# Performance work log

Measured on AMD Instinct MI355X. Metric: run time of the kernel, lower is better.

## Reference

```python
import jax, jax.numpy as jnp
import numpy as np

C = 4          # num_components
B = 2          # true batch
HEADS = 24
DIM_HEAD = 64
D = HEADS * DIM_HEAD      # 1536, attn.out_dim == query dim
CROSS = 2048              # encoder hidden dim
S = 2048                  # latent sequence length
E = 77                    # encoder sequence length
PAD = 77                  # pad_length (must equal E for the broadcast in the original code)


def setup_inputs() -> dict:
    key = jax.random.key(0)
    ks = jax.random.split(key, 12)
    w = 0.02
    return {
        "hidden_states": jax.random.normal(ks[0], (B * C, S, D), jnp.float32),
        "encoder_hidden_states": jax.random.normal(ks[1], (B * C, E, CROSS), jnp.float32),
        "Wq": jax.random.normal(ks[2], (D, D), jnp.float32) * w,
        "bq": jax.random.normal(ks[3], (D,), jnp.float32) * w,
        "Wk": jax.random.normal(ks[4], (D, CROSS), jnp.float32) * w,
        "bk": jax.random.normal(ks[5], (D,), jnp.float32) * w,
        "Wv": jax.random.normal(ks[6], (D, CROSS), jnp.float32) * w,
        "bv": jax.random.normal(ks[7], (D,), jnp.float32) * w,
        "Wo": jax.random.normal(ks[8], (D, D), jnp.float32) * w,
        "bo": jax.random.normal(ks[9], (D,), jnp.float32) * w,
        "pad_length": PAD,
    }


def reference(hidden_states, encoder_hidden_states, Wq, bq, Wk, bk, Wv, bv, Wo, bo, pad_length):
    BC, S_, D_ = hidden_states.shape
    E_ = encoder_hidden_states.shape[1]
    Bsz = BC // C
    scale = 1.0 / np.sqrt(DIM_HEAD)

    # projections (torch nn.Linear: x @ W.T + b)
    q = hidden_states @ Wq.T + bq                      # [BC, S, D]
    k = encoder_hidden_states @ Wk.T + bk              # [BC, E, D]
    v = encoder_hidden_states @ Wv.T + bv              # [BC, E, D]
    # pad branch: to_k/to_v applied to zeros -> just the bias, broadcast over pad tokens
    k_pad = jnp.broadcast_to(bk, (BC, pad_length, D_))  # [BC, PAD, D]
    v_pad = jnp.broadcast_to(bv, (BC, pad_length, D_))
    v = jnp.concatenate([v, v_pad], axis=1)            # [BC, E+PAD, D]

    # split heads
    qh = q.reshape(BC, S_, HEADS, DIM_HEAD)
    kh = k.reshape(BC, E_, HEADS, DIM_HEAD)
    kph = k_pad.reshape(BC, pad_length, HEADS, DIM_HEAD)
    vh = v.reshape(BC, E_ + pad_length, HEADS, DIM_HEAD)

    # scores: [BC, H, S, E] and [BC, H, S, PAD]
    scores = jnp.einsum("bihd,bjhd->bhij", qh, kh) * scale
    scores_pad = jnp.einsum("bihd,bjhd->bhij", qh, kph) * scale

    # component-wise softmax: view as [C, B, H, S, *], softmax over component axis 0
    scores = scores.reshape(C, Bsz, HEADS, S_, E_)
    scores_pad = scores_pad.reshape(C, Bsz, HEADS, S_, pad_length)
    w_main = jax.nn.softmax(scores, axis=0)
    w_pad = jax.nn.softmax(scores_pad, axis=0) * (C / pad_length) * (1.0 - w_main)

    w_main = w_main.reshape(BC, HEADS, S_, E_)
    w_pad = w_pad.reshape(BC, HEADS, S_, pad_length)
    weights = jnp.concatenate([w_main, w_pad], axis=-1)  # [BC, H, S, E+PAD]

    # attention @ V -> merge heads
    out = jnp.einsum("bhij,bjhd->bihd", weights, vh).reshape(BC, S_, D_)
    out = out @ Wo.T + bo   # to_out[0]; dropout is identity in eval
    return out
```

## Files before the change

### kernel.cpp

```cpp
#include <hip/hip_runtime.h>
#include <hip/hip_bf16.h>


typedef __attribute__((ext_vector_type(8))) short short8;
typedef __attribute__((ext_vector_type(4))) float f32x4;
typedef __attribute__((ext_vector_type(4))) _Float16 half4;

#define DEV __device__ __forceinline__

DEV ushort f2bf(float x) {
  __hip_bfloat16 h = __float2bfloat16(x);
  return *reinterpret_cast<ushort*>(&h);
}


__global__ __launch_bounds__(256) void cvt_all(const float* __restrict__ hs, ushort* __restrict__ hs_bf,
                                               const float* __restrict__ Wq, ushort* __restrict__ Wq_bf,
                                               const float* __restrict__ Wk, ushort* __restrict__ Wk_bf,
                                               const float* __restrict__ Wv, ushort* __restrict__ Wv_bf,
                                               const float* __restrict__ Wo, ushort* __restrict__ Wo_bf,
                                               const float* __restrict__ ehs, ushort* __restrict__ ehs_bf) {
  const int b0 = 6291456;
  const int b1 = b0 + 589824;
  const int b2 = b1 + 786432;
  const int b3 = b2 + 786432;
  const int b4 = b3 + 589824;
  const int total = b4 + 327680;
  int idx = blockIdx.x * blockDim.x + threadIdx.x;
  int stride = gridDim.x * blockDim.x;
  for (int q = idx; q < total; q += stride) {
    const float* in; ushort* out; int qq;
    bool zero = false;
    if (q < b0)      { in = hs;  out = hs_bf;  qq = q; }
    else if (q < b1) { in = Wq;  out = Wq_bf;  qq = q - b0; }
    else if (q < b2) { in = Wk;  out = Wk_bf;  qq = q - b1; }
    else if (q < b3) { in = Wv;  out = Wv_bf;  qq = q - b2; }
    else if (q < b4) { in = Wo;  out = Wo_bf;  qq = q - b3; }
    else {
      qq = q - b4;
      int r = qq >> 9;
      in = ehs; out = ehs_bf;
      zero = (r >= 616);
    }
    ushort4 o;
    if (!zero) {
      float4 f = reinterpret_cast<const float4*>(in)[qq];
      o.x = f2bf(f.x); o.y = f2bf(f.y); o.z = f2bf(f.z); o.w = f2bf(f.w);
    } else {
      o.x = 0; o.y = 0; o.z = 0; o.w = 0;
    }
    reinterpret_cast<ushort4*>(out)[qq] = o;
  }
}


template <typename OutT>
DEV void gemm_body(const ushort* __restrict__ A, const ushort* __restrict__ B,
                   const float* __restrict__ bias, OutT* __restrict__ C,
                   int M, int N, int K) {
  __shared__ __align__(16) ushort lds[32768];
  const int tid = threadIdx.x;
  const int lane = tid & 63;
  const int wid = tid >> 6;
  const int wr = wid >> 1, wc = wid & 1;

  const int nwg = gridDim.x * gridDim.y;
  const int lin = blockIdx.y * gridDim.x + blockIdx.x;
  const int q8 = nwg >> 3, r8 = nwg & 7;
  const int xcd = lin & 7, i8 = lin >> 3;
  const int swl = (xcd < r8 ? xcd * (q8 + 1) : r8 * (q8 + 1) + (xcd - r8) * q8) + i8;
  const long m0 = (long)(swl / gridDim.y) * 128;
  const long n0 = (long)(swl % gridDim.y) * 128;

  const int ll = lane & 15, g = lane >> 4;
  const int swz = ll & 7;

  const int srow = wid * 8 + (lane >> 3);
  const int scol = ((lane & 7) ^ (lane >> 3)) * 8;
  const ushort* pa = A + (m0 + srow) * (long)K + scol;
  const ushort* pb = B + (n0 + srow) * (long)K + scol;
  const long qstep = 32 * (long)K;

  f32x4 acc[4][4] = {};

#define STAGE(tt, bsel)                                                                    \
  do {                                                                                     \
    const long kt_ = (long)(tt) * 64;                                                      \
    const int ab_ = (bsel) * 32768 + wid * 1024;                                           \
    _Pragma("unroll") for (int q = 0; q < 4; ++q)                                          \
        __builtin_amdgcn_global_load_lds(                                                  \
            (const __attribute__((address_space(1))) void*)(pa + kt_ + q * qstep),         \
            (__attribute__((address_space(3))) void*)((char*)lds + ab_ + q * 4096),        \
            16, 0, 0);                                                                     \
    _Pragma("unroll") for (int q = 0; q < 4; ++q)                                          \
        __builtin_amdgcn_global_load_lds(                                                  \
            (const __attribute__((address_space(1))) void*)(pb + kt_ + q * qstep),         \
            (__attribute__((address_space(3))) void*)((char*)lds + ab_ + 16384 + q * 4096),\
            16, 0, 0);                                                                     \
  } while (0)

  const int nt = K >> 6;
  STAGE(0, 0);
  STAGE(1, 1);
  asm volatile("s_waitcnt vmcnt(8)" ::: "memory");
  __builtin_amdgcn_s_barrier();

  for (int t = 0; t < nt; ++t) {
    const int buf = t & 1;
    const char* abase = (const char*)lds + buf * 32768;
    const char* bbase = abase + 16384;
    short8 af[4][2], bfr[4][2];
#pragma unroll
    for (int m = 0; m < 4; ++m)
#pragma unroll
      for (int ks = 0; ks < 2; ++ks)
        af[m][ks] = *reinterpret_cast<const short8*>(
            abase + (wr * 64 + m * 16 + ll) * 128 + (((ks * 4 + g) ^ swz) * 16));
#pragma unroll
    for (int n = 0; n < 4; ++n)
#pragma unroll
      for (int ks = 0; ks < 2; ++ks)
        bfr[n][ks] = *reinterpret_cast<const short8*>(
            bbase + (wc * 64 + n * 16 + ll) * 128 + (((ks * 4 + g) ^ swz) * 16));
    asm volatile("s_waitcnt lgkmcnt(0)" ::: "memory");
    __builtin_amdgcn_s_barrier();

    if (t < nt - 2) {
      STAGE(t + 2, buf);
      asm volatile("s_waitcnt vmcnt(8)" ::: "memory");
    } else if (t == nt - 2) {
      asm volatile("s_waitcnt vmcnt(0)" ::: "memory");
    }
    __builtin_amdgcn_sched_barrier(0);
    __builtin_amdgcn_s_setprio(1);
#pragma unroll
    for (int ks = 0; ks < 2; ++ks)
#pragma unroll
      for (int m = 0; m < 4; ++m)
#pragma unroll
        for (int n = 0; n < 4; ++n)
          acc[m][n] =
              __builtin_amdgcn_mfma_f32_16x16x32_bf16(af[m][ks], bfr[n][ks], acc[m][n], 0, 0, 0);
    __builtin_amdgcn_s_setprio(0);
    __builtin_amdgcn_s_barrier();
  }
#undef STAGE

#pragma unroll
  for (int m = 0; m < 4; ++m) {
#pragma unroll
    for (int n = 0; n < 4; ++n) {
      const int row = wr * 64 + m * 16 + g * 4;
      const int col = wc * 64 + n * 16 + ll;
      const float bias_v = bias[n0 + col];
#pragma unroll
      for (int r = 0; r < 4; ++r) {
        float val = acc[m][n][r] + bias_v;
        long off = (m0 + row + r) * (long)N + n0 + col;
        if constexpr (sizeof(OutT) == 2) {
          C[off] = (OutT)f2bf(val);
        } else {
          C[off] = val;
        }
      }
    }
  }
}

template <typename OutT>
__global__ __launch_bounds__(256) void gemm_p(const ushort* __restrict__ A,
                                              const ushort* __restrict__ B,
                                              const float* __restrict__ bias,
                                              OutT* __restrict__ C, int M, int N, int K) {
  gemm_body<OutT>(A, B, bias, C, M, N, K);
}

__global__ __launch_bounds__(256) void gemm_p_kv(const ushort* __restrict__ A,
                                                 const ushort* __restrict__ Bk,
                                                 const float* __restrict__ bk, float* Ck,
                                                 const ushort* __restrict__ Bv,
                                                 const float* __restrict__ bv, float* Cv,
                                                 int M, int N, int K) {
  if (blockIdx.z == 0)
    gemm_body<float>(A, Bk, bk, Ck, M, N, K);
  else
    gemm_body<float>(A, Bv, bv, Cv, M, N, K);
}


__global__ __launch_bounds__(256) void prep_kv(const float* __restrict__ k_f,
                                               const float* __restrict__ v_f,
                                               const float* __restrict__ bk,
                                               const float* __restrict__ bv,
                                               ushort* __restrict__ kimg,
                                               ushort* __restrict__ vimg) {
  __shared__ _Float16 vl[80][68];
  const int c = blockIdx.x, h = blockIdx.y, bb = blockIdx.z;
  const int tid = threadIdx.x;
  const long ibase = ((long)(bb * 24 + h)) * 20480 + c * 5120;

  for (int rr = tid; rr < 640; rr += 256) {
    int j = rr >> 3, t = rr & 7;
    short8 v = {};
    const float* src = nullptr;
    if (j < 77)
      src = k_f + ((long)((c * 2 + bb) * 77 + j)) * 1536 + h * 64 + t * 8;
    else if (j == 77)
      src = bk + h * 64 + t * 8;
    if (src) {
      float4 f0 = reinterpret_cast<const float4*>(src)[0];
      float4 f1 = reinterpret_cast<const float4*>(src)[1];
      v[0] = f2bf(f0.x); v[1] = f2bf(f0.y); v[2] = f2bf(f0.z); v[3] = f2bf(f0.w);
      v[4] = f2bf(f1.x); v[5] = f2bf(f1.y); v[6] = f2bf(f1.z); v[7] = f2bf(f1.w);
    }
    *reinterpret_cast<short8*>(kimg + ibase + j * 64 + (t ^ (j & 7)) * 8) = v;
  }
  for (int rr = tid; rr < 640; rr += 256) {
    int j = rr >> 3, t = rr & 7;
    half4 lo = {}, hi = {};
    const float* src = nullptr;
    if (j < 77)
      src = v_f + ((long)((c * 2 + bb) * 77 + j)) * 1536 + h * 64 + t * 8;
    else if (j == 77)
      src = bv + h * 64 + t * 8;
    if (src) {
      float4 f0 = reinterpret_cast<const float4*>(src)[0];
      float4 f1 = reinterpret_cast<const float4*>(src)[1];
      lo[0] = (_Float16)f0.x; lo[1] = (_Float16)f0.y; lo[2] = (_Float16)f0.z; lo[3] = (_Float16)f0.w;
      hi[0] = (_Float16)f1.x; hi[1] = (_Float16)f1.y; hi[2] = (_Float16)f1.z; hi[3] = (_Float16)f1.w;
    }
    *reinterpret_cast<half4*>(&vl[j][t * 8]) = lo;
    *reinterpret_cast<half4*>(&vl[j][t * 8 + 4]) = hi;
  }
  __syncthreads();
  const int d = tid & 63, jg = tid >> 6;
  ushort* vrow = vimg + ibase + d * 80;
  const int x = (d >> 2) & 3;
#pragma unroll
  for (int b = 0; b < 5; ++b) {
    int jb = jg * 5 + b;
    half4 hv;
#pragma unroll
    for (int e = 0; e < 4; ++e) hv[e] = vl[jb * 4 + e][d];
    *reinterpret_cast<half4*>(vrow + ((jb ^ x) << 2)) = hv;
  }
}


__global__ __launch_bounds__(256) void attn_v4(const ushort* __restrict__ qg,
                                               const ushort* __restrict__ kimg,
                                               const ushort* __restrict__ vimg,
                                               ushort* __restrict__ ao) {
  __shared__ __align__(16) ushort vt[20480];
  const int tid = threadIdx.x;
  const int lane = tid & 63;
  const int w = tid >> 6;
  const int h = blockIdx.y, bb = blockIdx.z;
  const int i0 = blockIdx.x * 64;
  const long ib = ((long)(bb * 24 + h)) * 20480;

#pragma unroll
  for (int p = 0; p < 10; ++p) {
    int is = p * 4 + w;
    __builtin_amdgcn_global_load_lds(
        (const __attribute__((address_space(1))) void*)(vimg + ib + is * 512 + lane * 8),
        (__attribute__((address_space(3))) void*)((char*)vt + is * 1024), 16, 0, 0);
  }

  const int ll = lane & 15, g = lane >> 4;

  f32x4 s[4][5];
#pragma unroll
  for (int c = 0; c < 4; ++c)
#pragma unroll
    for (int m = 0; m < 5; ++m) s[c][m] = (f32x4){0.f, 0.f, 0.f, 0.f};

#pragma unroll
  for (int c = 0; c < 4; ++c) {
    const ushort* qbase =
        qg + ((long)((c * 2 + bb) * 2048 + i0 + w * 16 + ll)) * 1536 + h * 64 + g * 8;
    short8 qf0 = *reinterpret_cast<const short8*>(qbase);
    short8 qf1 = *reinterpret_cast<const short8*>(qbase + 32);
    const ushort* kbase = kimg + ib + c * 5120;
#pragma unroll
    for (int m = 0; m < 5; ++m) {
      const ushort* rb = kbase + (m * 16 + ll) * 64;
      short8 a0 = *reinterpret_cast<const short8*>(rb + (g ^ (ll & 7)) * 8);
      short8 a1 = *reinterpret_cast<const short8*>(rb + ((4 + g) ^ (ll & 7)) * 8);
      s[c][m] = __builtin_amdgcn_mfma_f32_16x16x32_bf16(a0, qf0, s[c][m], 0, 0, 0);
      s[c][m] = __builtin_amdgcn_mfma_f32_16x16x32_bf16(a1, qf1, s[c][m], 0, 0, 0);
    }
  }

  const float scale = 0.125f;
  float wsum0 = 0.f, wsum1 = 0.f, wsum2 = 0.f, wsum3 = 0.f;
#pragma unroll
  for (int m = 0; m < 5; ++m) {
#pragma unroll
    for (int e = 0; e < 4; ++e) {
      float x0 = s[0][m][e] * scale, x1 = s[1][m][e] * scale;
      float x2 = s[2][m][e] * scale, x3 = s[3][m][e] * scale;
      float mx = fmaxf(fmaxf(x0, x1), fmaxf(x2, x3));
      float e0 = __expf(x0 - mx), e1 = __expf(x1 - mx);
      float e2 = __expf(x2 - mx), e3 = __expf(x3 - mx);
      float inv = __fdividef(1.f, e0 + e1 + e2 + e3);
      float w0 = e0 * inv, w1 = e1 * inv, w2 = e2 * inv, w3 = e3 * inv;
      int jj = m * 16 + g * 4 + e;
      float msk = (jj < 77) ? 1.f : 0.f;
      wsum0 += w0 * msk; wsum1 += w1 * msk; wsum2 += w2 * msk; wsum3 += w3 * msk;
      s[0][m][e] = w0; s[1][m][e] = w1; s[2][m][e] = w2; s[3][m][e] = w3;
    }
  }
  wsum0 += __shfl_xor(wsum0, 16); wsum0 += __shfl_xor(wsum0, 32);
  wsum1 += __shfl_xor(wsum1, 16); wsum1 += __shfl_xor(wsum1, 32);
  wsum2 += __shfl_xor(wsum2, 16); wsum2 += __shfl_xor(wsum2, 32);
  wsum3 += __shfl_xor(wsum3, 16); wsum3 += __shfl_xor(wsum3, 32);

  const bool g3 = (g == 3);
  {
    float wsum[4] = {wsum0, wsum1, wsum2, wsum3};
#pragma unroll
    for (int c = 0; c < 4; ++c) {
      float w77 = s[c][4][1];
      float pwv = w77 * (4.0f / 77.0f) * (77.0f - wsum[c]);
      s[c][4][1] = g3 ? pwv : w77;
      s[c][4][2] = g3 ? 0.f : s[c][4][2];
      s[c][4][3] = g3 ? 0.f : s[c][4][3];
    }
  }

  half4 wf[4][5];
#pragma unroll
  for (int c = 0; c < 4; ++c)
#pragma unroll
    for (int m = 0; m < 5; ++m) {
      half4 hv;
      hv[0] = (_Float16)s[c][m][0];
      hv[1] = (_Float16)s[c][m][1];
      hv[2] = (_Float16)s[c][m][2];
      hv[3] = (_Float16)s[c][m][3];
      wf[c][m] = hv;
    }

  __syncthreads();

  f32x4 o[4][4];
#pragma unroll
  for (int c = 0; c < 4; ++c)
#pragma unroll
    for (int n = 0; n < 4; ++n) o[c][n] = (f32x4){0.f, 0.f, 0.f, 0.f};

#pragma unroll
  for (int c = 0; c < 4; ++c)
#pragma unroll
    for (int m = 0; m < 5; ++m)
#pragma unroll
      for (int n = 0; n < 4; ++n) {
        const int dd = n * 16 + ll;
        const int jb = (m * 4 + g) ^ ((dd >> 2) & 3);
        half4 vf = *reinterpret_cast<const half4*>(
            reinterpret_cast<const _Float16*>(vt) + c * 5120 + dd * 80 + (jb << 2));
        o[c][n] = __builtin_amdgcn_mfma_f32_16x16x16f16(wf[c][m], vf, o[c][n], 0, 0, 0);
      }

#pragma unroll
  for (int c = 0; c < 4; ++c)
#pragma unroll
    for (int n = 0; n < 4; ++n)
#pragma unroll
      for (int r = 0; r < 4; ++r) {
        long row = (long)((c * 2 + bb) * 2048 + i0 + w * 16 + g * 4 + r);
        ao[row * 1536 + h * 64 + n * 16 + ll] = f2bf(o[c][n][r]);
      }
}


extern "C" void kernel_launch(void* const* d_in, const int* in_sizes, int n_in,
                              void* d_out, int out_size, void* d_ws, size_t ws_size,
                              hipStream_t stream) {
  (void)in_sizes; (void)n_in; (void)out_size; (void)ws_size;
  const float* hs  = (const float*)d_in[0];
  const float* ehs = (const float*)d_in[1];
  const float* Wq  = (const float*)d_in[2];
  const float* bq  = (const float*)d_in[3];
  const float* Wk  = (const float*)d_in[4];
  const float* bk  = (const float*)d_in[5];
  const float* Wv  = (const float*)d_in[6];
  const float* bv  = (const float*)d_in[7];
  const float* Wo  = (const float*)d_in[8];
  const float* bo  = (const float*)d_in[9];
  float* out = (float*)d_out;

  char* ws = (char*)d_ws;
  size_t off = 0;
  auto alloc = [&](size_t bytes) {
    char* p = ws + off;
    off += (bytes + 255) & ~(size_t)255;
    return p;
  };
  ushort* hs_bf  = (ushort*)alloc(16384UL * 1536 * 2);
  ushort* ehs_bf = (ushort*)alloc(640UL * 2048 * 2);
  ushort* Wq_bf  = (ushort*)alloc(1536UL * 1536 * 2);
  ushort* Wk_bf  = (ushort*)alloc(1536UL * 2048 * 2);
  ushort* Wv_bf  = (ushort*)alloc(1536UL * 2048 * 2);
  ushort* Wo_bf  = (ushort*)alloc(1536UL * 1536 * 2);
  ushort* q_bf   = (ushort*)alloc(16384UL * 1536 * 2);
  float*  k_f    = (float*)alloc(640UL * 1536 * 4);
  float*  v_f    = (float*)alloc(640UL * 1536 * 4);
  ushort* ao_bf  = (ushort*)alloc(16384UL * 1536 * 2);
  ushort* kimg   = (ushort*)alloc(48UL * 20480 * 2);
  ushort* vimg   = (ushort*)alloc(48UL * 20480 * 2);

  dim3 b256(256);
  cvt_all<<<4096, b256, 0, stream>>>(hs, hs_bf, Wq, Wq_bf, Wk, Wk_bf, Wv, Wv_bf,
                                     Wo, Wo_bf, ehs, ehs_bf);

  gemm_p_kv<<<dim3(5, 12, 2), b256, 0, stream>>>(ehs_bf, Wk_bf, bk, k_f, Wv_bf, bv, v_f,
                                                 640, 1536, 2048);
  prep_kv<<<dim3(4, 24, 2), b256, 0, stream>>>(k_f, v_f, bk, bv, kimg, vimg);
  gemm_p<ushort><<<dim3(128, 12), b256, 0, stream>>>(hs_bf, Wq_bf, bq, q_bf, 16384, 1536, 1536);
  attn_v4<<<dim3(32, 24, 2), b256, 0, stream>>>(q_bf, kimg, vimg, ao_bf);
  gemm_p<float><<<dim3(128, 12), b256, 0, stream>>>(ao_bf, Wo_bf, bo, out, 16384, 1536, 1536);
}
```

Measured before the change: 265.8 us.

## Replace Q-projection GEMM with 8-wave 256x256 ping-pong pipelined kernel

Adds a new GEMM kernel for the Q projection with 512 threads and 256x256 output tiles. It double-buffers operands in 128KB of LDS via direct global-to-LDS loads, uses an XOR swizzle, and interleaves staging, LDS reads and MFMA phases with explicit barriers, waitcnts and priority hints. Blocks are remapped so that consecutive blocks are spread across XCDs. The aim is to keep the matrix units busy while memory traffic is hidden, at the cost of one block per CU and a fragile hand-scheduled pipeline that assumes K is a multiple of 128 and that M and N divide evenly by 256.

```diff
diff --git a/kernel.cpp b/kernel.cpp
--- a/kernel.cpp
+++ b/kernel.cpp
@@ -188,6 +188,155 @@
 }
 
 
+#define BAR8 __builtin_amdgcn_s_barrier()
+#define LGKM0_8 do { asm volatile("s_waitcnt lgkmcnt(0)" ::: "memory"); \
+                     __builtin_amdgcn_sched_barrier(0); } while (0)
+#define VMC(n_) do { asm volatile("s_waitcnt vmcnt(" #n_ ")" ::: "memory"); \
+                     __builtin_amdgcn_sched_barrier(0); } while (0)
+
+template <typename OutT>
+__global__ __launch_bounds__(512, 1) void gemm8p(const ushort* __restrict__ A,
+                                                 const ushort* __restrict__ B,
+                                                 const float* __restrict__ bias,
+                                                 OutT* __restrict__ C,
+                                                 int M, int N, int K, int nnx) {
+  extern __shared__ char dl[];
+  const int tid = threadIdx.x;
+  const int lane = tid & 63;
+  const int w = tid >> 6;
+  const int wr = w >> 2, wc = w & 3;
+  const int ll = lane & 15, g = lane >> 4;
+  const int swz = ll & 7;
+
+  const int cpx = gridDim.x >> 3;
+  const int sw = (blockIdx.x & 7) * cpx + (blockIdx.x >> 3);
+  const long m0 = (long)(sw / nnx) * 256;
+  const long n0 = (long)(sw % nnx) * 256;
+
+  const int srow = tid >> 3;
+  const int scol = ((tid & 7) ^ (srow & 7)) * 8;
+  const ushort* pa = A + (m0 + srow) * (long)K + scol;
+  const ushort* pb = B + (n0 + srow) * (long)K + scol;
+
+#define STG8(mat, tt, h, bf_)                                                              \
+  do {                                                                                     \
+    const ushort* s_ = ((mat) ? pb : pa) + (long)((h) * 128) * K + (long)(tt) * 64;        \
+    char* d_ = dl + (bf_) * 65536 + (mat) * 32768 + (h) * 16384 + tid * 16;                \
+    __builtin_amdgcn_global_load_lds((const __attribute__((address_space(1))) void*)s_,    \
+        (__attribute__((address_space(3))) void*)d_, 16, 0, 0);                            \
+    __builtin_amdgcn_global_load_lds(                                                      \
+        (const __attribute__((address_space(1))) void*)(s_ + 64 * (long)K),                \
+        (__attribute__((address_space(3))) void*)(d_ + 8192), 16, 0, 0);                   \
+  } while (0)
+
+#define RD_B8(bf_)                                                                         \
+  _Pragma("unroll") for (int n = 0; n < 4; ++n)                                            \
+  _Pragma("unroll") for (int k2 = 0; k2 < 2; ++k2)                                         \
+    bfr[n][k2] = *reinterpret_cast<const short8*>(                                         \
+        dl + (bf_) * 65536 + 32768 + (wc * 64 + n * 16 + ll) * 128 +                       \
+        (((k2 * 4 + g) ^ swz) * 16));
+
+#define RD_ALO8(bf_, k2)                                                                   \
+  _Pragma("unroll") for (int m = 0; m < 4; ++m)                                            \
+    aLo[m][k2] = *reinterpret_cast<const short8*>(                                         \
+        dl + (bf_) * 65536 + (wr * 128 + m * 16 + ll) * 128 +                              \
+        ((((k2) * 4 + g) ^ swz) * 16));
+
+#define RD_AHI8(bf_)                                                                       \
+  _Pragma("unroll") for (int m = 0; m < 4; ++m)                                            \
+  _Pragma("unroll") for (int k2 = 0; k2 < 2; ++k2)                                         \
+    aHi[m][k2] = *reinterpret_cast<const short8*>(                                         \
+        dl + (bf_) * 65536 + (wr * 128 + 64 + m * 16 + ll) * 128 +                         \
+        (((k2 * 4 + g) ^ swz) * 16));
+
+#define MF8(ab, areg, k2)                                                                  \
+  do {                                                                                     \
+    __builtin_amdgcn_s_setprio(1);                                                         \
+    _Pragma("unroll") for (int m = 0; m < 4; ++m)                                          \
+    _Pragma("unroll") for (int n = 0; n < 4; ++n)                                          \
+      acc[(ab) + m][n] = __builtin_amdgcn_mfma_f32_16x16x32_bf16(                          \
+          areg[m][k2], bfr[n][k2], acc[(ab) + m][n], 0, 0, 0);                             \
+    __builtin_amdgcn_s_setprio(0);                                                         \
+  } while (0)
+
+  f32x4 acc[8][4] = {};
+  short8 aLo[4][2], aHi[4][2], bfr[4][2];
+
+  const int nt = K >> 6;
+  STG8(1, 0, 0, 0); STG8(1, 0, 1, 0); STG8(0, 0, 0, 0); STG8(0, 0, 1, 0);
+  STG8(1, 1, 0, 1); STG8(1, 1, 1, 1); STG8(0, 1, 0, 1);
+  VMC(6);
+  BAR8;
+
+  const int iters = nt / 2 - 1;
+  for (int i = 0; i < iters; ++i) {
+    const int t = 2 * i;
+    RD_B8(0); RD_ALO8(0, 0);
+    STG8(0, t + 1, 1, 1);
+    BAR8; LGKM0_8; MF8(0, aLo, 0); BAR8;
+    RD_ALO8(0, 1); RD_AHI8(0);
+    STG8(1, t + 2, 0, 0);
+    BAR8; LGKM0_8; MF8(0, aLo, 1); BAR8;
+    STG8(1, t + 2, 1, 0);
+    BAR8; MF8(4, aHi, 0); BAR8;
+    STG8(0, t + 2, 0, 0);
+    VMC(6);
+    BAR8; MF8(4, aHi, 1); BAR8;
+    RD_B8(1); RD_ALO8(1, 0);
+    STG8(0, t + 2, 1, 0);
+    BAR8; LGKM0_8; MF8(0, aLo, 0); BAR8;
+    RD_ALO8(1, 1); RD_AHI8(1);
+    STG8(1, t + 3, 0, 1);
+    BAR8; LGKM0_8; MF8(0, aLo, 1); BAR8;
+    STG8(1, t + 3, 1, 1);
+    BAR8; MF8(4, aHi, 0); BAR8;
+    STG8(0, t + 3, 0, 1);
+    VMC(6);
+    BAR8; MF8(4, aHi, 1); BAR8;
+  }
+  RD_B8(0); RD_ALO8(0, 0);
+  STG8(0, nt - 1, 1, 1);
+  BAR8; LGKM0_8; MF8(0, aLo, 0); BAR8;
+  RD_ALO8(0, 1); RD_AHI8(0);
+  BAR8; LGKM0_8; MF8(0, aLo, 1); BAR8;
+  BAR8; MF8(4, aHi, 0); BAR8;
+  VMC(0);
+  BAR8; MF8(4, aHi, 1); BAR8;
+  RD_B8(1); RD_ALO8(1, 0);
+  BAR8; LGKM0_8; MF8(0, aLo, 0); BAR8;
+  RD_ALO8(1, 1); RD_AHI8(1);
+  BAR8; LGKM0_8; MF8(0, aLo, 1); BAR8;
+  MF8(4, aHi, 0);
+  MF8(4, aHi, 1);
+
+#undef STG8
+#undef RD_B8
+#undef RD_ALO8
+#undef RD_AHI8
+#undef MF8
+
+#pragma unroll
+  for (int m = 0; m < 8; ++m) {
+#pragma unroll
+    for (int n = 0; n < 4; ++n) {
+      const int row = wr * 128 + m * 16 + g * 4;
+      const int col = wc * 64 + n * 16 + ll;
+      const float bias_v = bias[n0 + col];
+#pragma unroll
+      for (int r = 0; r < 4; ++r) {
+        float val = acc[m][n][r] + bias_v;
+        long off = (m0 + row + r) * (long)N + n0 + col;
+        if constexpr (sizeof(OutT) == 2) {
+          C[off] = (OutT)f2bf(val);
+        } else {
+          C[off] = val;
+        }
+      }
+    }
+  }
+}
+
+
 __global__ __launch_bounds__(256) void prep_kv(const float* __restrict__ k_f,
                                                const float* __restrict__ v_f,
                                                const float* __restrict__ bk,
@@ -411,6 +560,9 @@
   ushort* kimg   = (ushort*)alloc(48UL * 20480 * 2);
   ushort* vimg   = (ushort*)alloc(48UL * 20480 * 2);
 
+  hipFuncSetAttribute(reinterpret_cast<const void*>(&gemm8p<ushort>),
+                      hipFuncAttributeMaxDynamicSharedMemorySize, 131072);
+
   dim3 b256(256);
   cvt_all<<<4096, b256, 0, stream>>>(hs, hs_bf, Wq, Wq_bf, Wk, Wk_bf, Wv, Wv_bf,
                                      Wo, Wo_bf, ehs, ehs_bf);
@@ -418,7 +570,7 @@
   gemm_p_kv<<<dim3(5, 12, 2), b256, 0, stream>>>(ehs_bf, Wk_bf, bk, k_f, Wv_bf, bv, v_f,
                                                  640, 1536, 2048);
   prep_kv<<<dim3(4, 24, 2), b256, 0, stream>>>(k_f, v_f, bk, bv, kimg, vimg);
-  gemm_p<ushort><<<dim3(128, 12), b256, 0, stream>>>(hs_bf, Wq_bf, bq, q_bf, 16384, 1536, 1536);
+  gemm8p<ushort><<<384, 512, 131072, stream>>>(hs_bf, Wq_bf, bq, q_bf, 16384, 1536, 1536, 6);
   attn_v4<<<dim3(32, 24, 2), b256, 0, stream>>>(q_bf, kimg, vimg, ao_bf);
   gemm_p<float><<<dim3(128, 12), b256, 0, stream>>>(ao_bf, Wo_bf, bo, out, 16384, 1536, 1536);
 }
```

Result: slower. 306.3 us (+15.3%).
